# Kernel tuning notes

Measured on AMD Instinct MI355X. Metric: run time of the kernel, lower is better.

## Reference

```python
import jax, jax.numpy as jnp
import numpy as np

QMIN_A, QMAX_A = -128, 127   # int8 activation range
QMIN_W, QMAX_W = -8, 7       # int4 weight range
EPS = float(np.finfo(np.float32).eps)


def per_token_dynamic_quant(x):
    """Asymmetric per-token int8 quantize -> dequantize (fake quant), matching torchao."""
    mn = jnp.minimum(jnp.min(x, axis=-1, keepdims=True), 0.0)
    mx = jnp.maximum(jnp.max(x, axis=-1, keepdims=True), 0.0)
    scale = jnp.maximum((mx - mn) / (QMAX_A - QMIN_A), EPS)
    zp = jnp.clip(QMIN_A - jnp.round(mn / scale), QMIN_A, QMAX_A)
    q = jnp.clip(jnp.round(x / scale) + zp, QMIN_A, QMAX_A)
    return (q - zp) * scale


def setup_inputs() -> dict:
    key = jax.random.key(0)
    k1, k2, k3, k4 = jax.random.split(key, 4)
    B, S, IN, OUT, G = 4, 2048, 4096, 4096, 256
    x = jax.random.normal(k1, (B, S, IN), dtype=jnp.float32)
    # int4 values stored in int8 container, range [-8, 7]
    weight_int8 = jax.random.randint(k2, (OUT, IN), QMIN_W, QMAX_W + 1, dtype=jnp.int32).astype(jnp.int8)
    scales = jax.random.uniform(k3, (OUT, IN // G), dtype=jnp.float32, minval=0.005, maxval=0.02)
    zeros = jnp.round(jax.random.uniform(k4, (OUT, IN // G), minval=-2.0, maxval=2.0)).astype(jnp.float32)
    bias = jax.random.normal(jax.random.fold_in(key, 7), (OUT,), dtype=jnp.float32) * 0.01
    return {"x": x, "weight_int8": weight_int8, "scales": scales, "zeros": zeros, "bias": bias}


def reference(x, weight_int8, scales, zeros, bias):
    O, I = weight_int8.shape
    G = I // scales.shape[1]
    xq = per_token_dynamic_quant(x)
    # groupwise int4 dequant: (w - zero_point) * scale per (1, G) block
    w = weight_int8.astype(jnp.float32).reshape(O, I // G, G)
    w_dq = ((w - zeros[:, :, None]) * scales[:, :, None]).reshape(O, I)
    return jnp.einsum('bsi,oi->bso', xq, w_dq) + bias
```

## Files before the change

kernel.cpp:

```cpp
#include <hip/hip_runtime.h>
#include <stdint.h>

typedef unsigned short ushort_t;
typedef __attribute__((ext_vector_type(4))) int   i32x4;
typedef __attribute__((ext_vector_type(16))) int  i32x16;

#define TM 128
#define TN 128
#define BKB 128


__device__ __forceinline__ void async16(const void* g, void* l) {
  __builtin_amdgcn_global_load_lds(
      (__attribute__((address_space(1))) void*)g,
      (__attribute__((address_space(3))) void*)l,
      16, 0, 0);
}

__device__ __forceinline__ int swz(int r) { return (r ^ (r >> 3)) & 7; }

__global__ __launch_bounds__(256) void quant_kernel(
    const float* __restrict__ x, int8_t* __restrict__ Aq,
    float* __restrict__ tokScale, float* __restrict__ tokZp, int K)
{
  const int token = blockIdx.x;
  const int t = threadIdx.x;
  const float4* xin = (const float4*)(x + (size_t)token * K);

  float4 v[4];
#pragma unroll
  for (int j = 0; j < 4; ++j) v[j] = xin[t + 256 * j];

  float mn = v[0].x, mx = v[0].x;
#pragma unroll
  for (int j = 0; j < 4; ++j) {
    mn = fminf(mn, fminf(fminf(v[j].x, v[j].y), fminf(v[j].z, v[j].w)));
    mx = fmaxf(mx, fmaxf(fmaxf(v[j].x, v[j].y), fmaxf(v[j].z, v[j].w)));
  }
#pragma unroll
  for (int off = 32; off >= 1; off >>= 1) {
    mn = fminf(mn, __shfl_xor(mn, off));
    mx = fmaxf(mx, __shfl_xor(mx, off));
  }

  __shared__ float smn[4], smx[4];
  const int wave = t >> 6, lane = t & 63;
  if (lane == 0) { smn[wave] = mn; smx[wave] = mx; }
  __syncthreads();
  mn = fminf(fminf(smn[0], smn[1]), fminf(smn[2], smn[3]));
  mx = fmaxf(fmaxf(smx[0], smx[1]), fmaxf(smx[2], smx[3]));

  mn = fminf(mn, 0.0f);
  mx = fmaxf(mx, 0.0f);
  const float scale = fmaxf((mx - mn) / 255.0f, 1.1920929e-07f);
  float zp = -128.0f - rintf(mn / scale);
  zp = fminf(fmaxf(zp, -128.0f), 127.0f);
  const float rs = 1.0f / scale;

  uint32_t* dst = (uint32_t*)(Aq + (size_t)token * K);
#pragma unroll
  for (int j = 0; j < 4; ++j) {
    float e[4] = {v[j].x, v[j].y, v[j].z, v[j].w};
    uint32_t pk = 0;
#pragma unroll
    for (int i = 0; i < 4; ++i) {
      float q = rintf(e[i] * rs) + zp;
      q = fminf(fmaxf(q, -128.0f), 127.0f);
      pk |= ((uint32_t)(int)q & 0xFFu) << (8 * i);
    }
    dst[t + 256 * j] = pk;
  }

  if (t == 0) { tokScale[token] = scale; tokZp[token] = zp; }
}

__global__ __launch_bounds__(256) void wprep_kernel(
    const int* __restrict__ W, const float* __restrict__ scales,
    const float* __restrict__ zeros, int8_t* __restrict__ Wq,
    float* __restrict__ T, int K, int gpr, int G)
{
  const int row = blockIdx.x;
  const int t = threadIdx.x;
  const int4* wp = (const int4*)(W + (size_t)row * K);
  uint32_t* dst = (uint32_t*)(Wq + (size_t)row * K);

  float partial = 0.0f;
#pragma unroll
  for (int j = 0; j < 4; ++j) {
    const int idx = t + 256 * j;
    const int g = (idx * 4) / G;
    const float s = scales[(size_t)row * gpr + g];
    const int zi = (int)zeros[(size_t)row * gpr + g];
    int4 w4 = wp[idx];
    const int a = w4.x - zi, b = w4.y - zi, c = w4.z - zi, d = w4.w - zi;
    dst[idx] = ((uint32_t)a & 0xFFu) | (((uint32_t)b & 0xFFu) << 8)
             | (((uint32_t)c & 0xFFu) << 16) | (((uint32_t)d & 0xFFu) << 24);
    partial += s * (float)(a + b + c + d);
  }

#pragma unroll
  for (int off = 32; off >= 1; off >>= 1) partial += __shfl_xor(partial, off);
  __shared__ float sp[4];
  const int wave = t >> 6, lane = t & 63;
  if (lane == 0) sp[wave] = partial;
  __syncthreads();
  if (t == 0) T[row] = (sp[0] + sp[1]) + (sp[2] + sp[3]);
}

__global__ __launch_bounds__(256) void gemm_kernel(
    const int8_t* __restrict__ A,
    const int8_t* __restrict__ B,
    const float* __restrict__ scales,
    const float* __restrict__ tokScale, const float* __restrict__ tokZp,
    const float* __restrict__ T, const float* __restrict__ bias,
    float* __restrict__ C, int M, int N, int K, int gpr)
{
  __shared__ __align__(16) int8_t As[TM * BKB];
  __shared__ __align__(16) int8_t Bs[TN * BKB];
  __shared__ float sS[16 * TN];

  const int tid   = threadIdx.x;
  const int lane  = tid & 63;
  const int wave  = tid >> 6;
  const int m0 = blockIdx.y * TM;
  const int n0 = blockIdx.x * TN;
  const int wm = (wave & 1) * 64;
  const int wn = (wave >> 1) * 64;
  const int col32 = lane & 31;
  const int khalf = lane >> 5;

  int rA[2], kA[2], rB[2], kB[2];
#pragma unroll
  for (int i = 0; i < 2; ++i) {
    rA[i] = wm + i * 32 + col32;  kA[i] = (rA[i] ^ (rA[i] >> 3)) & 7;
    rB[i] = wn + i * 32 + col32;  kB[i] = (rB[i] ^ (rB[i] >> 3)) & 7;
  }

#pragma unroll
  for (int jj = 0; jj < (16 * TN) / 256; ++jj) {
    const int flat = tid + 256 * jj;
    const int i = flat >> 4, g = flat & 15;
    sS[g * TN + i] = scales[(size_t)(n0 + i) * gpr + g];
  }

  float accf[2][2][16];
#pragma unroll
  for (int i = 0; i < 2; ++i)
#pragma unroll
    for (int j = 0; j < 2; ++j)
#pragma unroll
      for (int r = 0; r < 16; ++r) accf[i][j][r] = 0.0f;

  i32x16 zeroC;
#pragma unroll
  for (int r = 0; r < 16; ++r) zeroC[r] = 0;

  const int ngroups = K / 256;
  for (int g = 0; g < ngroups; ++g) {
    i32x16 ai[2][2];
#pragma unroll
    for (int half = 0; half < 2; ++half) {
      const int k0 = g * 256 + half * BKB;
#pragma unroll
      for (int it = 0; it < 4; ++it) {
        const int p = (it << 8) + tid;
        const int r = p >> 3;
        const int c = (p & 7) ^ ((r ^ (r >> 3)) & 7);
        const int ldsoff = it * 4096 + wave * 1024;
        async16(A + (size_t)(m0 + r) * K + k0 + (c << 4), &As[ldsoff]);
        async16(B + (size_t)(n0 + r) * K + k0 + (c << 4), &Bs[ldsoff]);
      }
      __syncthreads();

#pragma unroll
      for (int kk = 0; kk < 4; ++kk) {
        const int cw = kk * 2 + khalf;
        i32x4 af[2], bf[2];
#pragma unroll
        for (int i = 0; i < 2; ++i)
          af[i] = *(const i32x4*)&As[rA[i] * BKB + ((cw ^ kA[i]) << 4)];
#pragma unroll
        for (int j = 0; j < 2; ++j)
          bf[j] = *(const i32x4*)&Bs[rB[j] * BKB + ((cw ^ kB[j]) << 4)];
#pragma unroll
        for (int i = 0; i < 2; ++i)
#pragma unroll
          for (int j = 0; j < 2; ++j) {
            if (half == 0 && kk == 0)
              ai[i][j] = __builtin_amdgcn_mfma_i32_32x32x32_i8(af[i], bf[j], zeroC, 0, 0, 0);
            else
              ai[i][j] = __builtin_amdgcn_mfma_i32_32x32x32_i8(af[i], bf[j], ai[i][j], 0, 0, 0);
          }
      }
      __syncthreads();
    }
#pragma unroll
    for (int j = 0; j < 2; ++j) {
      const float s = sS[g * TN + wn + j * 32 + col32];
#pragma unroll
      for (int i = 0; i < 2; ++i)
#pragma unroll
        for (int r = 0; r < 16; ++r)
          accf[i][j][r] += s * (float)ai[i][j][r];
    }
  }

  int   nj[2];
  float Tn[2], bn[2];
#pragma unroll
  for (int j = 0; j < 2; ++j) {
    nj[j] = n0 + wn + j * 32 + col32;
    Tn[j] = T[nj[j]];
    bn[j] = bias[nj[j]];
  }
  const int rbase = 4 * khalf;
#pragma unroll
  for (int i = 0; i < 2; ++i) {
    const int mb = m0 + wm + i * 32;
#pragma unroll
    for (int r = 0; r < 16; ++r) {
      const int m = mb + (r & 3) + 8 * (r >> 2) + rbase;
      const float ts = tokScale[m];
      const float zp = tokZp[m];
      float* crow = C + (size_t)m * N;
#pragma unroll
      for (int j = 0; j < 2; ++j)
        crow[nj[j]] = ts * (accf[i][j][r] - zp * Tn[j]) + bn[j];
    }
  }
}

extern "C" void kernel_launch(void* const* d_in, const int* in_sizes, int n_in,
                              void* d_out, int out_size, void* d_ws, size_t ws_size,
                              hipStream_t stream) {
  const float* x      = (const float*)d_in[0];
  const int*   w      = (const int*)d_in[1];
  const float* scales = (const float*)d_in[2];
  const float* zeros  = (const float*)d_in[3];
  const float* bias   = (const float*)d_in[4];
  float* out = (float*)d_out;

  const int OUT = in_sizes[4];
  const int IN  = in_sizes[1] / OUT;
  const int M   = in_sizes[0] / IN;
  const int gpr = in_sizes[2] / OUT;
  const int G   = IN / gpr;

  int8_t* Aq = (int8_t*)d_ws;
  int8_t* Wq = Aq + (size_t)M * IN;
  float* tokScale = (float*)(Wq + (size_t)OUT * IN);
  float* tokZp = tokScale + M;
  float* T = tokZp + M;

  quant_kernel<<<M, 256, 0, stream>>>(x, Aq, tokScale, tokZp, IN);
  wprep_kernel<<<OUT, 256, 0, stream>>>(w, scales, zeros, Wq, T, IN, gpr, G);
  gemm_kernel<<<dim3(OUT / TN, M / TM), 256, 0, stream>>>(
      Aq, Wq, scales, tokScale, tokZp, T, bias, out, M, OUT, IN, gpr);
}
```

Baseline: 437.4 us.

## Pipeline int8 GEMM with 3-stage async LDS buffers, larger tile, merged prep kernels

The GEMM moves to a 256x128 tile with 512 threads and a three-stage global-to-LDS async buffer ring. Counted vmcnt waits let the next K-step's loads overlap the current MFMA work instead of draining with a full barrier each step. The activation-quant and weight-prep kernels are merged into one launch to save a kernel boundary. The cost is roughly 144KB of LDS per block, which limits occupancy, plus more fragile hand-written waitcnt synchronisation.

```diff
diff --git a/kernel.cpp b/kernel.cpp
--- a/kernel.cpp
+++ b/kernel.cpp
@@ -1,13 +1,13 @@
 #include <hip/hip_runtime.h>
 #include <stdint.h>
 
-typedef unsigned short ushort_t;
 typedef __attribute__((ext_vector_type(4))) int   i32x4;
 typedef __attribute__((ext_vector_type(16))) int  i32x16;
 
-#define TM 128
+#define TM 256
 #define TN 128
 #define BKB 128
+#define NSTAGE 3
 
 
 __device__ __forceinline__ void async16(const void* g, void* l) {
@@ -19,95 +19,88 @@
 
 __device__ __forceinline__ int swz(int r) { return (r ^ (r >> 3)) & 7; }
 
-__global__ __launch_bounds__(256) void quant_kernel(
+__global__ __launch_bounds__(256) void prep_kernel(
     const float* __restrict__ x, int8_t* __restrict__ Aq,
-    float* __restrict__ tokScale, float* __restrict__ tokZp, int K)
-{
-  const int token = blockIdx.x;
-  const int t = threadIdx.x;
-  const float4* xin = (const float4*)(x + (size_t)token * K);
-
-  float4 v[4];
-#pragma unroll
-  for (int j = 0; j < 4; ++j) v[j] = xin[t + 256 * j];
-
-  float mn = v[0].x, mx = v[0].x;
-#pragma unroll
-  for (int j = 0; j < 4; ++j) {
-    mn = fminf(mn, fminf(fminf(v[j].x, v[j].y), fminf(v[j].z, v[j].w)));
-    mx = fmaxf(mx, fmaxf(fmaxf(v[j].x, v[j].y), fmaxf(v[j].z, v[j].w)));
-  }
-#pragma unroll
-  for (int off = 32; off >= 1; off >>= 1) {
-    mn = fminf(mn, __shfl_xor(mn, off));
-    mx = fmaxf(mx, __shfl_xor(mx, off));
-  }
-
-  __shared__ float smn[4], smx[4];
-  const int wave = t >> 6, lane = t & 63;
-  if (lane == 0) { smn[wave] = mn; smx[wave] = mx; }
-  __syncthreads();
-  mn = fminf(fminf(smn[0], smn[1]), fminf(smn[2], smn[3]));
-  mx = fmaxf(fmaxf(smx[0], smx[1]), fmaxf(smx[2], smx[3]));
-
-  mn = fminf(mn, 0.0f);
-  mx = fmaxf(mx, 0.0f);
-  const float scale = fmaxf((mx - mn) / 255.0f, 1.1920929e-07f);
-  float zp = -128.0f - rintf(mn / scale);
-  zp = fminf(fmaxf(zp, -128.0f), 127.0f);
-  const float rs = 1.0f / scale;
-
-  uint32_t* dst = (uint32_t*)(Aq + (size_t)token * K);
-#pragma unroll
-  for (int j = 0; j < 4; ++j) {
-    float e[4] = {v[j].x, v[j].y, v[j].z, v[j].w};
-    uint32_t pk = 0;
-#pragma unroll
-    for (int i = 0; i < 4; ++i) {
-      float q = rintf(e[i] * rs) + zp;
-      q = fminf(fmaxf(q, -128.0f), 127.0f);
-      pk |= ((uint32_t)(int)q & 0xFFu) << (8 * i);
-    }
-    dst[t + 256 * j] = pk;
-  }
-
-  if (t == 0) { tokScale[token] = scale; tokZp[token] = zp; }
-}
-
-__global__ __launch_bounds__(256) void wprep_kernel(
+    float* __restrict__ tokScale, float* __restrict__ tokZp,
     const int* __restrict__ W, const float* __restrict__ scales,
     const float* __restrict__ zeros, int8_t* __restrict__ Wq,
-    float* __restrict__ T, int K, int gpr, int G)
+    float* __restrict__ T, int K, int M, int gpr, int G)
 {
-  const int row = blockIdx.x;
   const int t = threadIdx.x;
-  const int4* wp = (const int4*)(W + (size_t)row * K);
-  uint32_t* dst = (uint32_t*)(Wq + (size_t)row * K);
-
-  float partial = 0.0f;
-#pragma unroll
-  for (int j = 0; j < 4; ++j) {
-    const int idx = t + 256 * j;
-    const int g = (idx * 4) / G;
-    const float s = scales[(size_t)row * gpr + g];
-    const int zi = (int)zeros[(size_t)row * gpr + g];
-    int4 w4 = wp[idx];
-    const int a = w4.x - zi, b = w4.y - zi, c = w4.z - zi, d = w4.w - zi;
-    dst[idx] = ((uint32_t)a & 0xFFu) | (((uint32_t)b & 0xFFu) << 8)
-             | (((uint32_t)c & 0xFFu) << 16) | (((uint32_t)d & 0xFFu) << 24);
-    partial += s * (float)(a + b + c + d);
-  }
-
-#pragma unroll
-  for (int off = 32; off >= 1; off >>= 1) partial += __shfl_xor(partial, off);
-  __shared__ float sp[4];
   const int wave = t >> 6, lane = t & 63;
-  if (lane == 0) sp[wave] = partial;
-  __syncthreads();
-  if (t == 0) T[row] = (sp[0] + sp[1]) + (sp[2] + sp[3]);
-}
-
-__global__ __launch_bounds__(256) void gemm_kernel(
+  __shared__ float sA[4], sB[4];
+
+  if ((int)blockIdx.x < M) {
+    const int token = blockIdx.x;
+    const float4* xin = (const float4*)(x + (size_t)token * K);
+    float4 v[4];
+#pragma unroll
+    for (int j = 0; j < 4; ++j) v[j] = xin[t + 256 * j];
+
+    float mn = v[0].x, mx = v[0].x;
+#pragma unroll
+    for (int j = 0; j < 4; ++j) {
+      mn = fminf(mn, fminf(fminf(v[j].x, v[j].y), fminf(v[j].z, v[j].w)));
+      mx = fmaxf(mx, fmaxf(fmaxf(v[j].x, v[j].y), fmaxf(v[j].z, v[j].w)));
+    }
+#pragma unroll
+    for (int off = 32; off >= 1; off >>= 1) {
+      mn = fminf(mn, __shfl_xor(mn, off));
+      mx = fmaxf(mx, __shfl_xor(mx, off));
+    }
+    if (lane == 0) { sA[wave] = mn; sB[wave] = mx; }
+    __syncthreads();
+    mn = fminf(fminf(sA[0], sA[1]), fminf(sA[2], sA[3]));
+    mx = fmaxf(fmaxf(sB[0], sB[1]), fmaxf(sB[2], sB[3]));
+
+    mn = fminf(mn, 0.0f);
+    mx = fmaxf(mx, 0.0f);
+    const float scale = fmaxf((mx - mn) / 255.0f, 1.1920929e-07f);
+    float zp = -128.0f - rintf(mn / scale);
+    zp = fminf(fmaxf(zp, -128.0f), 127.0f);
+    const float rs = 1.0f / scale;
+
+    uint32_t* dst = (uint32_t*)(Aq + (size_t)token * K);
+#pragma unroll
+    for (int j = 0; j < 4; ++j) {
+      float e[4] = {v[j].x, v[j].y, v[j].z, v[j].w};
+      uint32_t pk = 0;
+#pragma unroll
+      for (int i = 0; i < 4; ++i) {
+        float q = rintf(e[i] * rs) + zp;
+        q = fminf(fmaxf(q, -128.0f), 127.0f);
+        pk |= ((uint32_t)(int)q & 0xFFu) << (8 * i);
+      }
+      dst[t + 256 * j] = pk;
+    }
+    if (t == 0) { tokScale[token] = scale; tokZp[token] = zp; }
+  } else {
+    const int row = blockIdx.x - M;
+    const int4* wp = (const int4*)(W + (size_t)row * K);
+    uint32_t* dst = (uint32_t*)(Wq + (size_t)row * K);
+
+    float partial = 0.0f;
+#pragma unroll
+    for (int j = 0; j < 4; ++j) {
+      const int idx = t + 256 * j;
+      const int g = (idx * 4) / G;
+      const float s = scales[(size_t)row * gpr + g];
+      const int zi = (int)zeros[(size_t)row * gpr + g];
+      int4 w4 = wp[idx];
+      const int a = w4.x - zi, b = w4.y - zi, c = w4.z - zi, d = w4.w - zi;
+      dst[idx] = ((uint32_t)a & 0xFFu) | (((uint32_t)b & 0xFFu) << 8)
+               | (((uint32_t)c & 0xFFu) << 16) | (((uint32_t)d & 0xFFu) << 24);
+      partial += s * (float)(a + b + c + d);
+    }
+#pragma unroll
+    for (int off = 32; off >= 1; off >>= 1) partial += __shfl_xor(partial, off);
+    if (lane == 0) sA[wave] = partial;
+    __syncthreads();
+    if (t == 0) T[row] = (sA[0] + sA[1]) + (sA[2] + sA[3]);
+  }
+}
+
+__global__ __launch_bounds__(512, 2) void gemm_kernel(
     const int8_t* __restrict__ A,
     const int8_t* __restrict__ B,
     const float* __restrict__ scales,
@@ -115,8 +108,8 @@
     const float* __restrict__ T, const float* __restrict__ bias,
     float* __restrict__ C, int M, int N, int K, int gpr)
 {
-  __shared__ __align__(16) int8_t As[TM * BKB];
-  __shared__ __align__(16) int8_t Bs[TN * BKB];
+  __shared__ __align__(16) int8_t As[NSTAGE][TM * BKB];
+  __shared__ __align__(16) int8_t Bs[NSTAGE][TN * BKB];
   __shared__ float sS[16 * TN];
 
   const int tid   = threadIdx.x;
@@ -124,21 +117,40 @@
   const int wave  = tid >> 6;
   const int m0 = blockIdx.y * TM;
   const int n0 = blockIdx.x * TN;
-  const int wm = (wave & 1) * 64;
-  const int wn = (wave >> 1) * 64;
+  const int wm = (wave & 3) * 64;
+  const int wn = (wave >> 2) * 64;
   const int col32 = lane & 31;
   const int khalf = lane >> 5;
 
-  int rA[2], kA[2], rB[2], kB[2];
+  int rAoff[2], kA[2], rBoff[2], kB[2];
 #pragma unroll
   for (int i = 0; i < 2; ++i) {
-    rA[i] = wm + i * 32 + col32;  kA[i] = (rA[i] ^ (rA[i] >> 3)) & 7;
-    rB[i] = wn + i * 32 + col32;  kB[i] = (rB[i] ^ (rB[i] >> 3)) & 7;
-  }
-
-#pragma unroll
-  for (int jj = 0; jj < (16 * TN) / 256; ++jj) {
-    const int flat = tid + 256 * jj;
+    const int rA = wm + i * 32 + col32; rAoff[i] = rA * BKB; kA[i] = swz(rA);
+    const int rB = wn + i * 32 + col32; rBoff[i] = rB * BKB; kB[i] = swz(rB);
+  }
+
+  const int8_t* aSrc[4]; int aLds[4];
+  const int8_t* bSrc[2]; int bLds[2];
+#pragma unroll
+  for (int it = 0; it < 4; ++it) {
+    const int p = (it << 9) | tid;
+    const int r = p >> 3;
+    const int c = (p & 7) ^ swz(r);
+    aSrc[it] = A + (size_t)(m0 + r) * K + (c << 4);
+    aLds[it] = it * 8192 + wave * 1024;
+  }
+#pragma unroll
+  for (int it = 0; it < 2; ++it) {
+    const int p = (it << 9) | tid;
+    const int r = p >> 3;
+    const int c = (p & 7) ^ swz(r);
+    bSrc[it] = B + (size_t)(n0 + r) * K + (c << 4);
+    bLds[it] = it * 8192 + wave * 1024;
+  }
+
+#pragma unroll
+  for (int jj = 0; jj < (16 * TN) / 512; ++jj) {
+    const int flat = tid + 512 * jj;
     const int i = flat >> 4, g = flat & 15;
     sS[g * TN + i] = scales[(size_t)(n0 + i) * gpr + g];
   }
@@ -154,56 +166,82 @@
   i32x16 zeroC;
 #pragma unroll
   for (int r = 0; r < 16; ++r) zeroC[r] = 0;
-
-  const int ngroups = K / 256;
+  i32x16 ai[2][2];
+
+  const int nsteps = K / BKB;
+  const int ngroups = nsteps / 2;
+
+#define STAGE(sb, tt) do {                                                   \
+    const size_t koff = (size_t)(tt) * BKB;                                  \
+    _Pragma("unroll")                                                        \
+    for (int it = 0; it < 4; ++it) async16(aSrc[it] + koff, &As[sb][aLds[it]]); \
+    _Pragma("unroll")                                                        \
+    for (int it = 0; it < 2; ++it) async16(bSrc[it] + koff, &Bs[sb][bLds[it]]); \
+  } while (0)
+
+#define COMPUTE(sb, FIRST) do {                                              \
+    __builtin_amdgcn_s_setprio(1);                                           \
+    _Pragma("unroll")                                                        \
+    for (int kk = 0; kk < 4; ++kk) {                                         \
+      const int cw = kk * 2 + khalf;                                         \
+      i32x4 af[2], bf[2];                                                    \
+      _Pragma("unroll")                                                      \
+      for (int i = 0; i < 2; ++i)                                            \
+        af[i] = *(const i32x4*)&As[sb][rAoff[i] + ((cw ^ kA[i]) << 4)];      \
+      _Pragma("unroll")                                                      \
+      for (int j = 0; j < 2; ++j)                                            \
+        bf[j] = *(const i32x4*)&Bs[sb][rBoff[j] + ((cw ^ kB[j]) << 4)];      \
+      _Pragma("unroll")                                                      \
+      for (int i = 0; i < 2; ++i)                                            \
+        _Pragma("unroll")                                                    \
+        for (int j = 0; j < 2; ++j) {                                        \
+          if (FIRST && kk == 0)                                              \
+            ai[i][j] = __builtin_amdgcn_mfma_i32_32x32x32_i8(af[i], bf[j], zeroC, 0, 0, 0); \
+          else                                                               \
+            ai[i][j] = __builtin_amdgcn_mfma_i32_32x32x32_i8(af[i], bf[j], ai[i][j], 0, 0, 0); \
+        }                                                                    \
+    }                                                                        \
+    __builtin_amdgcn_s_setprio(0);                                           \
+  } while (0)
+
+#define FIXUP(g) do {                                                        \
+    _Pragma("unroll")                                                        \
+    for (int j = 0; j < 2; ++j) {                                            \
+      const float s = sS[(g) * TN + wn + j * 32 + col32];                    \
+      _Pragma("unroll")                                                      \
+      for (int i = 0; i < 2; ++i)                                            \
+        _Pragma("unroll")                                                    \
+        for (int r = 0; r < 16; ++r)                                         \
+          accf[i][j][r] += s * (float)ai[i][j][r];                           \
+    }                                                                        \
+  } while (0)
+
+#define SYNC6() do { asm volatile("s_waitcnt vmcnt(6) lgkmcnt(0)" ::: "memory"); \
+                     __builtin_amdgcn_s_barrier(); } while (0)
+#define SYNC0() do { asm volatile("s_waitcnt vmcnt(0) lgkmcnt(0)" ::: "memory"); \
+                     __builtin_amdgcn_s_barrier(); } while (0)
+
+  STAGE(0, 0);
+  STAGE(1, 1);
+  asm volatile("s_waitcnt vmcnt(6) lgkmcnt(0)" ::: "memory");
+  __builtin_amdgcn_s_barrier();
+
+  int b0 = 0, b1 = 1, b2 = 2;
   for (int g = 0; g < ngroups; ++g) {
-    i32x16 ai[2][2];
-#pragma unroll
-    for (int half = 0; half < 2; ++half) {
-      const int k0 = g * 256 + half * BKB;
-#pragma unroll
-      for (int it = 0; it < 4; ++it) {
-        const int p = (it << 8) + tid;
-        const int r = p >> 3;
-        const int c = (p & 7) ^ ((r ^ (r >> 3)) & 7);
-        const int ldsoff = it * 4096 + wave * 1024;
-        async16(A + (size_t)(m0 + r) * K + k0 + (c << 4), &As[ldsoff]);
-        async16(B + (size_t)(n0 + r) * K + k0 + (c << 4), &Bs[ldsoff]);
-      }
-      __syncthreads();
-
-#pragma unroll
-      for (int kk = 0; kk < 4; ++kk) {
-        const int cw = kk * 2 + khalf;
-        i32x4 af[2], bf[2];
-#pragma unroll
-        for (int i = 0; i < 2; ++i)
-          af[i] = *(const i32x4*)&As[rA[i] * BKB + ((cw ^ kA[i]) << 4)];
-#pragma unroll
-        for (int j = 0; j < 2; ++j)
-          bf[j] = *(const i32x4*)&Bs[rB[j] * BKB + ((cw ^ kB[j]) << 4)];
-#pragma unroll
-        for (int i = 0; i < 2; ++i)
-#pragma unroll
-          for (int j = 0; j < 2; ++j) {
-            if (half == 0 && kk == 0)
-              ai[i][j] = __builtin_amdgcn_mfma_i32_32x32x32_i8(af[i], bf[j], zeroC, 0, 0, 0);
-            else
-              ai[i][j] = __builtin_amdgcn_mfma_i32_32x32x32_i8(af[i], bf[j], ai[i][j], 0, 0, 0);
-          }
-      }
-      __syncthreads();
-    }
-#pragma unroll
-    for (int j = 0; j < 2; ++j) {
-      const float s = sS[g * TN + wn + j * 32 + col32];
-#pragma unroll
-      for (int i = 0; i < 2; ++i)
-#pragma unroll
-        for (int r = 0; r < 16; ++r)
-          accf[i][j][r] += s * (float)ai[i][j][r];
-    }
-  }
+    const int t = 2 * g;
+    if (t + 2 < nsteps) { STAGE(b2, t + 2); COMPUTE(b0, true); SYNC6(); }
+    else                {                   COMPUTE(b0, true); SYNC0(); }
+    if (t + 3 < nsteps)      { STAGE(b0, t + 3); COMPUTE(b1, false); FIXUP(g); SYNC6(); }
+    else if (t + 2 < nsteps) {                   COMPUTE(b1, false); FIXUP(g); SYNC0(); }
+    else                     {                   COMPUTE(b1, false); FIXUP(g); }
+    const int tmp = b0; b0 = b2; b2 = b1; b1 = tmp;
+  }
+
+#undef STAGE
+#undef COMPUTE
+#undef FIXUP
+#undef SYNC6
+#undef SYNC0
 
   int   nj[2];
   float Tn[2], bn[2];
@@ -252,8 +290,8 @@
   float* tokZp = tokScale + M;
   float* T = tokZp + M;
 
-  quant_kernel<<<M, 256, 0, stream>>>(x, Aq, tokScale, tokZp, IN);
-  wprep_kernel<<<OUT, 256, 0, stream>>>(w, scales, zeros, Wq, T, IN, gpr, G);
-  gemm_kernel<<<dim3(OUT / TN, M / TM), 256, 0, stream>>>(
+  prep_kernel<<<M + OUT, 256, 0, stream>>>(x, Aq, tokScale, tokZp,
+                                           w, scales, zeros, Wq, T, IN, M, gpr, G);
+  gemm_kernel<<<dim3(OUT / TN, M / TM), 512, 0, stream>>>(
       Aq, Wq, scales, tokScale, tokZp, T, bias, out, M, OUT, IN, gpr);
 }
```

New measurement: 459.8 us. 5.1% more time.
